# Optimization experiments

Measured on AMD Instinct MI355X. Metric: run time of the kernel, lower is better.

The kernel has to match this reference:

```python
import jax, jax.numpy as jnp
import numpy as np

N_NODES = 50000
N_EDGES = 1_000_000
N_HYPER = 1024
F_IN = 128
F_EDGE = 64


def setup_inputs() -> dict:
    key = jax.random.key(0)
    ks = jax.random.split(key, 20)
    s = 0.05
    return {
        "x": jax.random.normal(ks[0], (N_NODES, F_IN), jnp.float32),
        "edge_index": jax.random.randint(ks[1], (2, N_EDGES), 0, N_NODES, dtype=jnp.int64),
        "edge_weight": jax.random.uniform(ks[2], (N_EDGES,), jnp.float32),
        "edge_features": jax.random.normal(ks[3], (N_HYPER, F_EDGE), jnp.float32),
        "adj_e": jax.random.uniform(ks[4], (N_HYPER, N_HYPER), jnp.float32) / N_HYPER,
        "T": jax.random.uniform(ks[5], (N_NODES, N_HYPER), jnp.float32) / N_HYPER,
        # HypergraphConvLayer 1: 128 -> 64
        "W1": jax.random.normal(ks[6], (F_IN, 64), jnp.float32) * s,
        "b1": jnp.zeros((64,), jnp.float32),
        # HypergraphConvLayer 2: 64 -> 32
        "W2": jax.random.normal(ks[7], (64, 32), jnp.float32) * s,
        "b2": jnp.zeros((32,), jnp.float32),
        # GraphConvolution (CensNet-style): node 32->32, edge 64->32
        "Wn": jax.random.normal(ks[8], (32, 32), jnp.float32) * s,
        "We": jax.random.normal(ks[9], (F_EDGE, 32), jnp.float32) * s,
        "bg": jnp.zeros((32,), jnp.float32),
        # class_classifier: Linear(32,32) -> ReLU -> Linear(32,2) -> Softmax
        "Wc1": jax.random.normal(ks[10], (32, 32), jnp.float32) * s,
        "bc1": jnp.zeros((32,), jnp.float32),
        "Wc2": jax.random.normal(ks[11], (32, 2), jnp.float32) * s,
        "bc2": jnp.zeros((2,), jnp.float32),
    }


def _hconv(h, W, b, src, dst, edge_weight, num_nodes):
    # linear projection then edge-weighted scatter-add: out[dst] += w * h[src]
    h = h @ W + b
    msg = h[src] * edge_weight[:, None]          # [E, d]
    return jax.ops.segment_sum(msg, dst, num_segments=num_nodes)


def reference(x, edge_index, edge_weight, edge_features, adj_e, T,
              W1, b1, W2, b2, Wn, We, bg, Wc1, bc1, Wc2, bc2):
    n = x.shape[0]
    src, dst = edge_index[0], edge_index[1]

    h = jax.nn.relu(_hconv(x, W1, b1, src, dst, edge_weight, n))   # [N,64]
    h = jax.nn.relu(_hconv(h, W2, b2, src, dst, edge_weight, n))   # [N,32]

    # aggregate_node_features: node_features[dst] += h[src]; / num_edges
    num_edges = edge_index.shape[1]
    node_features = jax.ops.segment_sum(h[src], dst, num_segments=n) / num_edges

    # edge_conv: node linear + incidence-weighted hyperedge convolution
    edge_h = adj_e @ (edge_features @ We)                           # [NE,32]
    shared = jax.nn.relu(node_features @ Wn + T @ edge_h + bg)      # [N,32]

    # class_classifier
    c = jax.nn.relu(shared @ Wc1 + bc1)
    logits = c @ Wc2 + bc2
    return jax.nn.softmax(logits, axis=1)                           # [N,2]
```

## Files before the change

### kernel.cpp

```cpp
#include <hip/hip_runtime.h>
#include <hip/hip_bf16.h>

#define RPB 256

template<int COLS, int K>
__global__ __launch_bounds__(256) void gemm_k(
    const float* __restrict__ X, const float* __restrict__ W,
    const float* __restrict__ bias, float* __restrict__ out,
    int nrows, float scale, int relu_in)
{
    constexpr int CPT = COLS / 8;
    constexpr int KT  = 32;
    constexpr int NKT = K / KT;

    __shared__ float sx[RPB * 36];
    __shared__ float sWT[COLS * 33];

    const int tid = threadIdx.x;
    const int cg  = tid & 7;
    const int rg  = tid >> 3;
    const int r0  = blockIdx.x * RPB;

    float acc[8][CPT];
    #pragma unroll
    for (int r = 0; r < 8; ++r)
        #pragma unroll
        for (int c = 0; c < CPT; ++c) acc[r][c] = 0.f;

    for (int kt = 0; kt < NKT; ++kt) {
        #pragma unroll
        for (int j = 0; j < 8; ++j) {
            int i  = tid + j * 256;
            int r  = i >> 3;
            int k4 = i & 7;
            int gr = r0 + r; if (gr >= nrows) gr = nrows - 1;
            float4 v = *(const float4*)&X[(size_t)gr * K + kt * KT + k4 * 4];
            if (relu_in) {
                v.x = fmaxf(v.x, 0.f); v.y = fmaxf(v.y, 0.f);
                v.z = fmaxf(v.z, 0.f); v.w = fmaxf(v.w, 0.f);
            }
            if (scale != 1.f) { v.x *= scale; v.y *= scale; v.z *= scale; v.w *= scale; }
            *(float4*)&sx[r * 36 + k4 * 4] = v;
        }
        for (int i = tid; i < COLS * KT; i += 256) {
            int kl = i / COLS, c = i % COLS;
            sWT[c * 33 + kl] = W[(size_t)(kt * KT + kl) * COLS + c];
        }
        __syncthreads();

        #pragma unroll
        for (int k4 = 0; k4 < 8; ++k4) {
            float4 a[8];
            #pragma unroll
            for (int r = 0; r < 8; ++r)
                a[r] = *(const float4*)&sx[(r * 32 + rg) * 36 + k4 * 4];
            #pragma unroll
            for (int cc = 0; cc < CPT; ++cc) {
                int c = cg * CPT + cc;
                float w0 = sWT[c * 33 + k4 * 4 + 0];
                float w1 = sWT[c * 33 + k4 * 4 + 1];
                float w2 = sWT[c * 33 + k4 * 4 + 2];
                float w3 = sWT[c * 33 + k4 * 4 + 3];
                #pragma unroll
                for (int r = 0; r < 8; ++r)
                    acc[r][cc] += a[r].x * w0 + a[r].y * w1 + a[r].z * w2 + a[r].w * w3;
            }
        }
        __syncthreads();
    }

    #pragma unroll
    for (int r = 0; r < 8; ++r) {
        int row = r0 + r * 32 + rg;
        if (row < nrows) {
            #pragma unroll
            for (int cc4 = 0; cc4 < CPT / 4; ++cc4) {
                int c = cg * CPT + cc4 * 4;
                float4 o;
                o.x = acc[r][cc4 * 4 + 0] + (bias ? bias[c + 0] : 0.f);
                o.y = acc[r][cc4 * 4 + 1] + (bias ? bias[c + 1] : 0.f);
                o.z = acc[r][cc4 * 4 + 2] + (bias ? bias[c + 2] : 0.f);
                o.w = acc[r][cc4 * 4 + 3] + (bias ? bias[c + 3] : 0.f);
                *(float4*)&out[(size_t)row * COLS + c] = o;
            }
        }
    }
}

__global__ __launch_bounds__(256, 4) void tgemm2_k(
    const float* __restrict__ T, const float* __restrict__ eh,
    float* __restrict__ par, int nrows)
{
    __shared__ float seh[256 * 32];
    const int tid = threadIdx.x;
    const int ks  = blockIdx.y * 256;

    #pragma unroll
    for (int j = 0; j < 8; ++j) {
        int i = tid + j * 256;
        *(float4*)&seh[i * 4] = *(const float4*)&eh[(size_t)ks * 32 + (size_t)i * 4];
    }
    __syncthreads();

    int row = blockIdx.x * 256 + tid;
    int r   = row < nrows ? row : nrows - 1;
    const float* Tp = T + (size_t)r * 1024 + ks;

    float acc[32];
    #pragma unroll
    for (int c = 0; c < 32; ++c) acc[c] = 0.f;

    float4 t[8];
    #pragma unroll
    for (int q = 0; q < 8; ++q) t[q] = *(const float4*)&Tp[q * 4];

    for (int kc = 0; kc < 8; ++kc) {
        float4 tn[8];
        if (kc < 7) {
            #pragma unroll
            for (int q = 0; q < 8; ++q)
                tn[q] = *(const float4*)&Tp[(kc + 1) * 32 + q * 4];
        }
        #pragma unroll
        for (int q = 0; q < 8; ++q) {
            #pragma unroll
            for (int j = 0; j < 4; ++j) {
                float a = (j == 0) ? t[q].x : (j == 1) ? t[q].y : (j == 2) ? t[q].z : t[q].w;
                int k = kc * 32 + q * 4 + j;
                #pragma unroll
                for (int c4 = 0; c4 < 8; ++c4) {
                    float4 w = *(const float4*)&seh[k * 32 + c4 * 4];
                    acc[c4 * 4 + 0] += a * w.x;
                    acc[c4 * 4 + 1] += a * w.y;
                    acc[c4 * 4 + 2] += a * w.z;
                    acc[c4 * 4 + 3] += a * w.w;
                }
            }
        }
        #pragma unroll
        for (int q = 0; q < 8; ++q) t[q] = tn[q];
    }

    if (row < nrows) {
        float* p = par + (size_t)blockIdx.y * nrows * 32 + (size_t)row * 32;
        #pragma unroll
        for (int c4 = 0; c4 < 8; ++c4)
            *(float4*)&p[c4 * 4] = make_float4(acc[c4 * 4 + 0], acc[c4 * 4 + 1],
                                               acc[c4 * 4 + 2], acc[c4 * 4 + 3]);
    }
}

__global__ __launch_bounds__(256) void classify_k(
    const float* __restrict__ par, const float* __restrict__ nfw,
    const float* __restrict__ bg, const float* __restrict__ Wc1,
    const float* __restrict__ bc1, const float* __restrict__ Wc2,
    const float* __restrict__ bc2, float* __restrict__ out, int nrows)
{
    __shared__ float sWc1T[1024];
    __shared__ float sWc2[64];
    __shared__ float sb[66];

    int tid = threadIdx.x;
    for (int i = tid; i < 1024; i += 256)
        sWc1T[(i & 31) * 32 + (i >> 5)] = Wc1[i];
    if (tid < 64) sWc2[tid] = Wc2[tid];
    if (tid < 32)      sb[tid] = bc1[tid];
    else if (tid < 64) sb[tid] = bg[tid - 32];
    else if (tid < 66) sb[tid] = bc2[tid - 64];
    __syncthreads();

    int row = blockIdx.x * 256 + tid;
    if (row >= nrows) return;

    size_t stride = (size_t)nrows * 32;
    float4 sh4[8];
    #pragma unroll
    for (int i4 = 0; i4 < 8; ++i4) {
        const float* base = par + (size_t)row * 32 + i4 * 4;
        float4 v0 = *(const float4*)(base);
        float4 v1 = *(const float4*)(base + stride);
        float4 v2 = *(const float4*)(base + 2 * stride);
        float4 v3 = *(const float4*)(base + 3 * stride);
        float4 nf = *(const float4*)&nfw[(size_t)row * 32 + i4 * 4];
        float4 o;
        o.x = fmaxf(v0.x + v1.x + v2.x + v3.x + nf.x + sb[32 + i4 * 4 + 0], 0.f);
        o.y = fmaxf(v0.y + v1.y + v2.y + v3.y + nf.y + sb[32 + i4 * 4 + 1], 0.f);
        o.z = fmaxf(v0.z + v1.z + v2.z + v3.z + nf.z + sb[32 + i4 * 4 + 2], 0.f);
        o.w = fmaxf(v0.w + v1.w + v2.w + v3.w + nf.w + sb[32 + i4 * 4 + 3], 0.f);
        sh4[i4] = o;
    }

    float l0 = sb[64], l1 = sb[65];
    #pragma unroll
    for (int jj = 0; jj < 32; ++jj) {
        float s = sb[jj];
        #pragma unroll
        for (int i4 = 0; i4 < 8; ++i4) {
            float4 w4 = *(const float4*)&sWc1T[jj * 32 + i4 * 4];
            s += sh4[i4].x * w4.x + sh4[i4].y * w4.y
               + sh4[i4].z * w4.z + sh4[i4].w * w4.w;
        }
        s = fmaxf(s, 0.f);
        l0 += s * sWc2[jj * 2 + 0];
        l1 += s * sWc2[jj * 2 + 1];
    }
    float p0 = 1.f / (1.f + expf(l1 - l0));
    float p1 = 1.f / (1.f + expf(l0 - l1));
    *(float2*)&out[(size_t)row * 2] = make_float2(p0, p1);
}

__global__ void hist_k(const int* __restrict__ dst, int* __restrict__ deg, int E)
{
    int e = blockIdx.x * 256 + threadIdx.x;
    if (e < E) atomicAdd(&deg[dst[e]], 1);
}

__global__ void scan1_k(const int* __restrict__ deg, int* __restrict__ bsum, int N)
{
    __shared__ int s[256];
    int t = threadIdx.x, i = blockIdx.x * 256 + t;
    s[t] = (i < N) ? deg[i] : 0;
    __syncthreads();
    for (int off = 128; off > 0; off >>= 1) {
        if (t < off) s[t] += s[t + off];
        __syncthreads();
    }
    if (t == 0) bsum[blockIdx.x] = s[0];
}

__global__ void scan2_k(const int* __restrict__ bsum, int* __restrict__ boff,
                        int NB, int* __restrict__ rsN)
{
    __shared__ int s[256];
    int t = threadIdx.x;
    int v = (t < NB) ? bsum[t] : 0;
    s[t] = v;
    __syncthreads();
    for (int off = 1; off < 256; off <<= 1) {
        int u = (t >= off) ? s[t - off] : 0;
        __syncthreads();
        s[t] += u;
        __syncthreads();
    }
    if (t < NB) boff[t] = s[t] - v;
    if (t == NB - 1) *rsN = s[t];
}

__global__ void scan3_k(const int* __restrict__ deg, const int* __restrict__ boff,
                        int* __restrict__ rs, int* __restrict__ cur, int N)
{
    __shared__ int s[256];
    int t = threadIdx.x, i = blockIdx.x * 256 + t;
    int v = (i < N) ? deg[i] : 0;
    s[t] = v;
    __syncthreads();
    for (int off = 1; off < 256; off <<= 1) {
        int u = (t >= off) ? s[t - off] : 0;
        __syncthreads();
        s[t] += u;
        __syncthreads();
    }
    if (i < N) {
        int ex = boff[blockIdx.x] + s[t] - v;
        rs[i] = ex;
        cur[i] = ex;
    }
}

__global__ void fill_k(const int* __restrict__ src, const int* __restrict__ dst,
                       const float* __restrict__ ew, int* __restrict__ cur,
                       int* __restrict__ esrc, float* __restrict__ ews, int E)
{
    int e = blockIdx.x * 256 + threadIdx.x;
    if (e < E) {
        int pos = atomicAdd(&cur[dst[e]], 1);
        esrc[pos] = src[e];
        ews[pos]  = ew[e];
    }
}

__global__ __launch_bounds__(256) void gather64_k(
    const float* __restrict__ hp, const int* __restrict__ esrc,
    const float* __restrict__ ews, const int* __restrict__ rs,
    float* __restrict__ outv, int N)
{
    int lane = threadIdx.x & 63;
    int sub  = lane >> 4;
    int ch   = lane & 15;
    int wid  = (blockIdx.x * blockDim.x + threadIdx.x) >> 6;
    int nw   = (gridDim.x * blockDim.x) >> 6;
    for (int n = wid; n < N; n += nw) {
        int j0 = rs[n], j1 = rs[n + 1];
        float4 acc = make_float4(0.f, 0.f, 0.f, 0.f);
        for (int j = j0; j < j1; j += 8) {
            int ja = j + sub, jb = j + 4 + sub;
            bool va = ja < j1, vb = jb < j1;
            int ia = va ? ja : j0, ib = vb ? jb : j0;
            int sa = esrc[ia], sb2 = esrc[ib];
            float wa = va ? ews[ia] : 0.f;
            float wb = vb ? ews[ib] : 0.f;
            float4 v1 = *(const float4*)&hp[(size_t)sa * 64 + ch * 4];
            float4 v2 = *(const float4*)&hp[(size_t)sb2 * 64 + ch * 4];
            acc.x += v1.x * wa + v2.x * wb;
            acc.y += v1.y * wa + v2.y * wb;
            acc.z += v1.z * wa + v2.z * wb;
            acc.w += v1.w * wa + v2.w * wb;
        }
        acc.x += __shfl_xor(acc.x, 16); acc.y += __shfl_xor(acc.y, 16);
        acc.z += __shfl_xor(acc.z, 16); acc.w += __shfl_xor(acc.w, 16);
        acc.x += __shfl_xor(acc.x, 32); acc.y += __shfl_xor(acc.y, 32);
        acc.z += __shfl_xor(acc.z, 32); acc.w += __shfl_xor(acc.w, 32);
        if (lane < 16)
            *(float4*)&outv[(size_t)n * 64 + ch * 4] = acc;
    }
}

template<bool WEIGHTED, bool RELU>
__global__ __launch_bounds__(256) void gather32_k(
    const float* __restrict__ hp, const int* __restrict__ esrc,
    const float* __restrict__ ews, const int* __restrict__ rs,
    float* __restrict__ outv, int N)
{
    int lane = threadIdx.x & 63;
    int sub  = lane >> 3;
    int ch   = lane & 7;
    int wid  = (blockIdx.x * blockDim.x + threadIdx.x) >> 6;
    int nw   = (gridDim.x * blockDim.x) >> 6;
    for (int n = wid; n < N; n += nw) {
        int j0 = rs[n], j1 = rs[n + 1];
        float4 acc = make_float4(0.f, 0.f, 0.f, 0.f);
        for (int j = j0; j < j1; j += 16) {
            int ja = j + sub, jb = j + 8 + sub;
            bool va = ja < j1, vb = jb < j1;
            int ia = va ? ja : j0, ib = vb ? jb : j0;
            int sa = esrc[ia], sb2 = esrc[ib];
            float wa = WEIGHTED ? ews[ia] : 1.f;
            float wb = WEIGHTED ? ews[ib] : 1.f;
            if (!va) wa = 0.f;
            if (!vb) wb = 0.f;
            float4 v1 = *(const float4*)&hp[(size_t)sa * 32 + ch * 4];
            float4 v2 = *(const float4*)&hp[(size_t)sb2 * 32 + ch * 4];
            if (RELU) {
                v1.x = fmaxf(v1.x, 0.f); v1.y = fmaxf(v1.y, 0.f);
                v1.z = fmaxf(v1.z, 0.f); v1.w = fmaxf(v1.w, 0.f);
                v2.x = fmaxf(v2.x, 0.f); v2.y = fmaxf(v2.y, 0.f);
                v2.z = fmaxf(v2.z, 0.f); v2.w = fmaxf(v2.w, 0.f);
            }
            acc.x += v1.x * wa + v2.x * wb;
            acc.y += v1.y * wa + v2.y * wb;
            acc.z += v1.z * wa + v2.z * wb;
            acc.w += v1.w * wa + v2.w * wb;
        }
        acc.x += __shfl_xor(acc.x, 8);  acc.y += __shfl_xor(acc.y, 8);
        acc.z += __shfl_xor(acc.z, 8);  acc.w += __shfl_xor(acc.w, 8);
        acc.x += __shfl_xor(acc.x, 16); acc.y += __shfl_xor(acc.y, 16);
        acc.z += __shfl_xor(acc.z, 16); acc.w += __shfl_xor(acc.w, 16);
        acc.x += __shfl_xor(acc.x, 32); acc.y += __shfl_xor(acc.y, 32);
        acc.z += __shfl_xor(acc.z, 32); acc.w += __shfl_xor(acc.w, 32);
        if (lane < 8)
            *(float4*)&outv[(size_t)n * 32 + ch * 4] = acc;
    }
}

__global__ void efwe_k(const float* __restrict__ ef, const float* __restrict__ We,
                       float* __restrict__ tmp)
{
    int idx = blockIdx.x * 256 + threadIdx.x;
    int row = idx >> 5, c = idx & 31;
    float s = 0.f;
    #pragma unroll
    for (int k = 0; k < 64; ++k)
        s += ef[row * 64 + k] * We[k * 32 + c];
    tmp[row * 32 + c] = s;
}

__global__ void adjmm_k(const float* __restrict__ adj, const float* __restrict__ tmp,
                        float* __restrict__ edge_h)
{
    int kq     = blockIdx.x & 3;
    int rowblk = blockIdx.x >> 2;
    int r = rowblk * 8 + (threadIdx.x >> 5);
    int c = threadIdx.x & 31;
    float s = 0.f;
    int k0 = kq * 256;
    #pragma unroll 8
    for (int k = k0; k < k0 + 256; ++k)
        s += adj[r * 1024 + k] * tmp[k * 32 + c];
    atomicAdd(&edge_h[r * 32 + c], s);
}

extern "C" void kernel_launch(void* const* d_in, const int* in_sizes, int n_in,
                              void* d_out, int out_size, void* d_ws, size_t ws_size,
                              hipStream_t stream)
{
    const float* x   = (const float*)d_in[0];
    const int*   ei  = (const int*)  d_in[1];
    const float* ew  = (const float*)d_in[2];
    const float* ef  = (const float*)d_in[3];
    const float* adj = (const float*)d_in[4];
    const float* T   = (const float*)d_in[5];
    const float* W1  = (const float*)d_in[6];
    const float* b1  = (const float*)d_in[7];
    const float* W2  = (const float*)d_in[8];
    const float* b2  = (const float*)d_in[9];
    const float* Wn  = (const float*)d_in[10];
    const float* We  = (const float*)d_in[11];
    const float* bg  = (const float*)d_in[12];
    const float* Wc1 = (const float*)d_in[13];
    const float* bc1 = (const float*)d_in[14];
    const float* Wc2 = (const float*)d_in[15];
    const float* bc2 = (const float*)d_in[16];
    float* out = (float*)d_out;

    const int N = in_sizes[0] / 128;
    const int E = in_sizes[1] / 2;
    const int* srcIdx = ei;
    const int* dstIdx = ei + E;

    float* ws = (float*)d_ws;
    size_t o = 0;
    float* h1acc  = ws + o; o += (size_t)N * 64;
    float* h2acc  = ws + o; o += (size_t)N * 32;
    float* nfacc  = ws + o; o += (size_t)N * 32;
    float* edge_h = ws + o; o += 1024 * 32;
    float* tmp    = ws + o; o += 1024 * 32;
    float* nfw    = ws + o; o += (size_t)N * 32;
    float* par    = ws + o; o += (size_t)N * 128;
    float* h1p    = par;
    float* h2p    = par + (size_t)N * 64;
    int*   esrc   = (int*)(ws + o);   o += E;
    float* ews    = ws + o;           o += E;
    int*   deg    = (int*)(ws + o);   o += N;
    int*   rs     = (int*)(ws + o);   o += N + 1;
    int*   cur    = (int*)(ws + o);   o += N + 1;
    int*   bsum   = (int*)(ws + o);   o += 256;
    int*   boff   = (int*)(ws + o);   o += 256;

    const int NB = (N + 255) / 256;

    (void)hipMemsetAsync(deg, 0, (size_t)N * sizeof(int), stream);
    (void)hipMemsetAsync(edge_h, 0, 1024 * 32 * sizeof(float), stream);

    gemm_k<64, 128><<<NB, 256, 0, stream>>>(x, W1, b1, h1p, N, 1.f, 0);

    hist_k<<<(E + 255) / 256, 256, 0, stream>>>(dstIdx, deg, E);
    scan1_k<<<NB, 256, 0, stream>>>(deg, bsum, N);
    scan2_k<<<1, 256, 0, stream>>>(bsum, boff, NB, rs + N);
    scan3_k<<<NB, 256, 0, stream>>>(deg, boff, rs, cur, N);
    fill_k<<<(E + 255) / 256, 256, 0, stream>>>(srcIdx, dstIdx, ew, cur, esrc, ews, E);

    gather64_k<<<1024, 256, 0, stream>>>(h1p, esrc, ews, rs, h1acc, N);

    gemm_k<32, 64><<<NB, 256, 0, stream>>>(h1acc, W2, b2, h2p, N, 1.f, 1);

    gather32_k<true, false><<<1024, 256, 0, stream>>>(h2p, esrc, ews, rs, h2acc, N);

    gather32_k<false, true><<<1024, 256, 0, stream>>>(h2acc, esrc, ews, rs, nfacc, N);

    efwe_k<<<128, 256, 0, stream>>>(ef, We, tmp);
    adjmm_k<<<512, 256, 0, stream>>>(adj, tmp, edge_h);

    gemm_k<32, 32><<<NB, 256, 0, stream>>>(nfacc, Wn, nullptr, nfw, N, 1.f / (float)E, 0);

    tgemm2_k<<<dim3(NB, 4), 256, 0, stream>>>(T, edge_h, par, N);

    classify_k<<<NB, 256, 0, stream>>>(par, nfw, bg, Wc1, bc1, Wc2, bc2, out, N);
}
```

Before: 745.6 us.

## Pack CSR edge src/weight into int2 and map gathers to one thread-group per node

The fill kernel now writes each edge's source index and weight as one interleaved int2, so the gathers issue a single 8-byte load per edge instead of two separate loads. The three gather kernels drop the grid-stride wave-per-node scheme with intra-wave shuffle reductions. Each node is now handled by 16 (or 8) consecutive threads, each owning a float4 channel slice and looping over all of the node's edges serially, with the grid sized to cover every node. This removes the shuffle reductions and masked padding lanes, but each thread walks the whole neighbour list sequentially (about 20 edges on average), which gives less memory-level parallelism per node.

```diff
diff --git a/kernel.cpp b/kernel.cpp
--- a/kernel.cpp
+++ b/kernel.cpp
@@ -269,97 +269,58 @@
 
 __global__ void fill_k(const int* __restrict__ src, const int* __restrict__ dst,
                        const float* __restrict__ ew, int* __restrict__ cur,
-                       int* __restrict__ esrc, float* __restrict__ ews, int E)
+                       int2* __restrict__ epk, int E)
 {
     int e = blockIdx.x * 256 + threadIdx.x;
     if (e < E) {
         int pos = atomicAdd(&cur[dst[e]], 1);
-        esrc[pos] = src[e];
-        ews[pos]  = ew[e];
+        epk[pos] = make_int2(src[e], __float_as_int(ew[e]));
     }
 }
 
 __global__ __launch_bounds__(256) void gather64_k(
-    const float* __restrict__ hp, const int* __restrict__ esrc,
-    const float* __restrict__ ews, const int* __restrict__ rs,
-    float* __restrict__ outv, int N)
-{
-    int lane = threadIdx.x & 63;
-    int sub  = lane >> 4;
-    int ch   = lane & 15;
-    int wid  = (blockIdx.x * blockDim.x + threadIdx.x) >> 6;
-    int nw   = (gridDim.x * blockDim.x) >> 6;
-    for (int n = wid; n < N; n += nw) {
-        int j0 = rs[n], j1 = rs[n + 1];
-        float4 acc = make_float4(0.f, 0.f, 0.f, 0.f);
-        for (int j = j0; j < j1; j += 8) {
-            int ja = j + sub, jb = j + 4 + sub;
-            bool va = ja < j1, vb = jb < j1;
-            int ia = va ? ja : j0, ib = vb ? jb : j0;
-            int sa = esrc[ia], sb2 = esrc[ib];
-            float wa = va ? ews[ia] : 0.f;
-            float wb = vb ? ews[ib] : 0.f;
-            float4 v1 = *(const float4*)&hp[(size_t)sa * 64 + ch * 4];
-            float4 v2 = *(const float4*)&hp[(size_t)sb2 * 64 + ch * 4];
-            acc.x += v1.x * wa + v2.x * wb;
-            acc.y += v1.y * wa + v2.y * wb;
-            acc.z += v1.z * wa + v2.z * wb;
-            acc.w += v1.w * wa + v2.w * wb;
-        }
-        acc.x += __shfl_xor(acc.x, 16); acc.y += __shfl_xor(acc.y, 16);
-        acc.z += __shfl_xor(acc.z, 16); acc.w += __shfl_xor(acc.w, 16);
-        acc.x += __shfl_xor(acc.x, 32); acc.y += __shfl_xor(acc.y, 32);
-        acc.z += __shfl_xor(acc.z, 32); acc.w += __shfl_xor(acc.w, 32);
-        if (lane < 16)
-            *(float4*)&outv[(size_t)n * 64 + ch * 4] = acc;
-    }
+    const float* __restrict__ hp, const int2* __restrict__ epk,
+    const int* __restrict__ rs, float* __restrict__ outv, int N)
+{
+    int t = blockIdx.x * 256 + threadIdx.x;
+    if (t >= N * 16) return;
+    int n  = t >> 4;
+    int ch = t & 15;
+    int j0 = rs[n], j1 = rs[n + 1];
+    float4 acc = make_float4(0.f, 0.f, 0.f, 0.f);
+    for (int j = j0; j < j1; ++j) {
+        int2 e = epk[j];
+        float w = __int_as_float(e.y);
+        float4 v = *(const float4*)&hp[(size_t)e.x * 64 + ch * 4];
+        acc.x += v.x * w; acc.y += v.y * w;
+        acc.z += v.z * w; acc.w += v.w * w;
+    }
+    *(float4*)&outv[(size_t)n * 64 + ch * 4] = acc;
 }
 
 template<bool WEIGHTED, bool RELU>
 __global__ __launch_bounds__(256) void gather32_k(
-    const float* __restrict__ hp, const int* __restrict__ esrc,
-    const float* __restrict__ ews, const int* __restrict__ rs,
-    float* __restrict__ outv, int N)
-{
-    int lane = threadIdx.x & 63;
-    int sub  = lane >> 3;
-    int ch   = lane & 7;
-    int wid  = (blockIdx.x * blockDim.x + threadIdx.x) >> 6;
-    int nw   = (gridDim.x * blockDim.x) >> 6;
-    for (int n = wid; n < N; n += nw) {
-        int j0 = rs[n], j1 = rs[n + 1];
-        float4 acc = make_float4(0.f, 0.f, 0.f, 0.f);
-        for (int j = j0; j < j1; j += 16) {
-            int ja = j + sub, jb = j + 8 + sub;
-            bool va = ja < j1, vb = jb < j1;
-            int ia = va ? ja : j0, ib = vb ? jb : j0;
-            int sa = esrc[ia], sb2 = esrc[ib];
-            float wa = WEIGHTED ? ews[ia] : 1.f;
-            float wb = WEIGHTED ? ews[ib] : 1.f;
-            if (!va) wa = 0.f;
-            if (!vb) wb = 0.f;
-            float4 v1 = *(const float4*)&hp[(size_t)sa * 32 + ch * 4];
-            float4 v2 = *(const float4*)&hp[(size_t)sb2 * 32 + ch * 4];
-            if (RELU) {
-                v1.x = fmaxf(v1.x, 0.f); v1.y = fmaxf(v1.y, 0.f);
-                v1.z = fmaxf(v1.z, 0.f); v1.w = fmaxf(v1.w, 0.f);
-                v2.x = fmaxf(v2.x, 0.f); v2.y = fmaxf(v2.y, 0.f);
-                v2.z = fmaxf(v2.z, 0.f); v2.w = fmaxf(v2.w, 0.f);
-            }
-            acc.x += v1.x * wa + v2.x * wb;
-            acc.y += v1.y * wa + v2.y * wb;
-            acc.z += v1.z * wa + v2.z * wb;
-            acc.w += v1.w * wa + v2.w * wb;
-        }
-        acc.x += __shfl_xor(acc.x, 8);  acc.y += __shfl_xor(acc.y, 8);
-        acc.z += __shfl_xor(acc.z, 8);  acc.w += __shfl_xor(acc.w, 8);
-        acc.x += __shfl_xor(acc.x, 16); acc.y += __shfl_xor(acc.y, 16);
-        acc.z += __shfl_xor(acc.z, 16); acc.w += __shfl_xor(acc.w, 16);
-        acc.x += __shfl_xor(acc.x, 32); acc.y += __shfl_xor(acc.y, 32);
-        acc.z += __shfl_xor(acc.z, 32); acc.w += __shfl_xor(acc.w, 32);
-        if (lane < 8)
-            *(float4*)&outv[(size_t)n * 32 + ch * 4] = acc;
-    }
+    const float* __restrict__ hp, const int2* __restrict__ epk,
+    const int* __restrict__ rs, float* __restrict__ outv, int N)
+{
+    int t = blockIdx.x * 256 + threadIdx.x;
+    if (t >= N * 8) return;
+    int n  = t >> 3;
+    int ch = t & 7;
+    int j0 = rs[n], j1 = rs[n + 1];
+    float4 acc = make_float4(0.f, 0.f, 0.f, 0.f);
+    for (int j = j0; j < j1; ++j) {
+        int2 e = epk[j];
+        float w = WEIGHTED ? __int_as_float(e.y) : 1.f;
+        float4 v = *(const float4*)&hp[(size_t)e.x * 32 + ch * 4];
+        if (RELU) {
+            v.x = fmaxf(v.x, 0.f); v.y = fmaxf(v.y, 0.f);
+            v.z = fmaxf(v.z, 0.f); v.w = fmaxf(v.w, 0.f);
+        }
+        acc.x += v.x * w; acc.y += v.y * w;
+        acc.z += v.z * w; acc.w += v.w * w;
+    }
+    *(float4*)&outv[(size_t)n * 32 + ch * 4] = acc;
 }
 
 __global__ void efwe_k(const float* __restrict__ ef, const float* __restrict__ We,
@@ -428,8 +389,7 @@
     float* par    = ws + o; o += (size_t)N * 128;
     float* h1p    = par;
     float* h2p    = par + (size_t)N * 64;
-    int*   esrc   = (int*)(ws + o);   o += E;
-    float* ews    = ws + o;           o += E;
+    int2*  epk    = (int2*)(ws + o);  o += (size_t)E * 2;
     int*   deg    = (int*)(ws + o);   o += N;
     int*   rs     = (int*)(ws + o);   o += N + 1;
     int*   cur    = (int*)(ws + o);   o += N + 1;
@@ -447,15 +407,15 @@
     scan1_k<<<NB, 256, 0, stream>>>(deg, bsum, N);
     scan2_k<<<1, 256, 0, stream>>>(bsum, boff, NB, rs + N);
     scan3_k<<<NB, 256, 0, stream>>>(deg, boff, rs, cur, N);
-    fill_k<<<(E + 255) / 256, 256, 0, stream>>>(srcIdx, dstIdx, ew, cur, esrc, ews, E);
-
-    gather64_k<<<1024, 256, 0, stream>>>(h1p, esrc, ews, rs, h1acc, N);
+    fill_k<<<(E + 255) / 256, 256, 0, stream>>>(srcIdx, dstIdx, ew, cur, epk, E);
+
+    gather64_k<<<(N * 16 + 255) / 256, 256, 0, stream>>>(h1p, epk, rs, h1acc, N);
 
     gemm_k<32, 64><<<NB, 256, 0, stream>>>(h1acc, W2, b2, h2p, N, 1.f, 1);
 
-    gather32_k<true, false><<<1024, 256, 0, stream>>>(h2p, esrc, ews, rs, h2acc, N);
-
-    gather32_k<false, true><<<1024, 256, 0, stream>>>(h2acc, esrc, ews, rs, nfacc, N);
+    gather32_k<true, false><<<(N * 8 + 255) / 256, 256, 0, stream>>>(h2p, epk, rs, h2acc, N);
+
+    gather32_k<false, true><<<(N * 8 + 255) / 256, 256, 0, stream>>>(h2acc, epk, rs, nfacc, N);
 
     efwe_k<<<128, 256, 0, stream>>>(ef, We, tmp);
     adjmm_k<<<512, 256, 0, stream>>>(adj, tmp, edge_h);
```

Result: faster. 702.8 us (-5.8%).
